# Kernel optimization log

Measured on AMD Instinct MI355X. Metric: run time of the kernel, lower is better.

## Reference

```python
import jax, jax.numpy as jnp
import numpy as np

B, TQ, TK = 2, 2048, 2048
H, E, D = 16, 256, 4096       # num_heads, embed_dim, d_model
DH = D // H                   # head_dim == embed_dim (required by per-head RMSNorm(embed_dim))
LAMBDA_INIT = 0.8
LAYER_INDEX = 0
EPS = 1.1920929e-07           # torch RMSNorm default eps = finfo(float32).eps


def setup_inputs() -> dict:
    key = jax.random.key(0)
    ks = jax.random.split(key, 14)
    s = 0.02
    lam_init_val = LAMBDA_INIT - 0.6 * float(np.exp(-0.3 * LAYER_INDEX))
    return {
        "x": jax.random.normal(ks[0], (B, TQ, E), jnp.float32),
        "encoder_out": jax.random.normal(ks[1], (B, TK, E), jnp.float32),
        "Wq": jax.random.normal(ks[2], (H, E, DH), jnp.float32) * s,
        "bq": jnp.zeros((H, DH), jnp.float32),
        "Wk": jax.random.normal(ks[3], (H, E, DH), jnp.float32) * s,
        "bk": jnp.zeros((H, DH), jnp.float32),
        "Wv": jax.random.normal(ks[4], (H, E, DH), jnp.float32) * s,
        "bv": jnp.zeros((H, DH), jnp.float32),
        "lq1": jax.random.normal(ks[5], (H, DH), jnp.float32) * 0.1,
        "lk1": jax.random.normal(ks[6], (H, DH), jnp.float32) * 0.1,
        "lq2": jax.random.normal(ks[7], (H, DH), jnp.float32) * 0.1,
        "lk2": jax.random.normal(ks[8], (H, DH), jnp.float32) * 0.1,
        "lam_init": jnp.full((H,), lam_init_val, jnp.float32),
        "g": jnp.ones((H, DH), jnp.float32),     # per-head RMSNorm weight
        "Wo": jax.random.normal(ks[9], (D, E), jnp.float32) * s,
        "bo": jnp.zeros((E,), jnp.float32),
    }


def reference(x, encoder_out, Wq, bq, Wk, bk, Wv, bv,
              lq1, lk1, lq2, lk2, lam_init, g, Wo, bo):
    # per-head projections, vectorized over heads: [B,H,T,DH]
    q = jnp.einsum('bte,hed->bhtd', x, Wq) + bq[:, None, :]
    k = jnp.einsum('bse,hed->bhsd', encoder_out, Wk) + bk[:, None, :]
    v = jnp.einsum('bse,hed->bhsd', encoder_out, Wv) + bv[:, None, :]
    dh2 = DH // 2
    q1, q2 = q[..., :dh2], q[..., dh2:]
    k1, k2 = k[..., :dh2], k[..., dh2:]
    scale = 1.0 / jnp.sqrt(jnp.float32(dh2))
    s1 = jax.nn.softmax(jnp.einsum('bhtd,bhsd->bhts', q1, k1) * scale, axis=-1)
    s2 = jax.nn.softmax(jnp.einsum('bhtd,bhsd->bhts', q2, k2) * scale, axis=-1)
    # learned per-head lambda scalar
    lam = jnp.exp(jnp.sum(lq1 * lk1, axis=-1)) - jnp.exp(jnp.sum(lq2 * lk2, axis=-1)) + lam_init  # [H]
    w = s1 - lam[None, :, None, None] * s2
    o = jnp.einsum('bhts,bhsd->bhtd', w, v)
    # per-head RMSNorm + (1 - lambda_init) scaling
    rms = jnp.sqrt(jnp.mean(o * o, axis=-1, keepdims=True) + EPS)
    o = (1.0 - LAMBDA_INIT) * (o / rms) * g[None, :, None, :]
    # concat heads -> output projection
    o = o.transpose(0, 2, 1, 3).reshape(B, TQ, D)
    return o @ Wo + bo
```

## Files before the change

### kernel.cpp

```cpp
#include <hip/hip_runtime.h>
#include <hip/hip_bf16.h>
#include <stdint.h>
#include <math.h>

typedef __bf16 bf16;
typedef __bf16 bf16x8 __attribute__((ext_vector_type(8)));
typedef float f32x4 __attribute__((ext_vector_type(4)));
typedef float f32x16 __attribute__((ext_vector_type(16)));
typedef unsigned int u32;

#define MFMA16(a, b, c) __builtin_amdgcn_mfma_f32_16x16x32_bf16(a, b, c, 0, 0, 0)
#define MFMA32(a, b, c) __builtin_amdgcn_mfma_f32_32x32x16_bf16(a, b, c, 0, 0, 0)

typedef const u32 __attribute__((address_space(1)))* gptr1;
typedef u32 __attribute__((address_space(3)))* lptr3;

__device__ __forceinline__ void load_lds16(const void* g, void* l) {
    __builtin_amdgcn_global_load_lds((gptr1)g, (lptr3)l, 16, 0, 0);
}

__device__ __forceinline__ u32 pk2(float lo, float hi_) {
    union { bf16 h[2]; u32 u; } t;
    t.h[0] = (bf16)lo; t.h[1] = (bf16)hi_;
    return t.u;
}

#define SCALE_QK 0.08838834764831845f
#define LOG2E 1.4426950408889634f
#define QK_PRESCALE (SCALE_QK * LOG2E)
#define RMS_EPS 1.1920929e-07f
#define OUT_SCALE 0.2f
#define M0_BIAS (-16.0f)

__global__ void cvt_act(const float* __restrict__ x, const float* __restrict__ enc,
                        bf16* __restrict__ xb, bf16* __restrict__ eb) {
    int gid = blockIdx.x * 256 + threadIdx.x;
    const float* src = (gid < 131072) ? x : enc;
    bf16* dst = (gid < 131072) ? xb : eb;
    int i = (gid & 131071) * 8;
    float4 v0 = *(const float4*)(src + i);
    float4 v1 = *(const float4*)(src + i + 4);
    union { bf16 h[8]; uint4 u; } p;
    p.h[0] = (bf16)v0.x; p.h[1] = (bf16)v0.y; p.h[2] = (bf16)v0.z; p.h[3] = (bf16)v0.w;
    p.h[4] = (bf16)v1.x; p.h[5] = (bf16)v1.y; p.h[6] = (bf16)v1.z; p.h[7] = (bf16)v1.w;
    *(uint4*)(dst + i) = p.u;
}

__global__ void txp_w(const float* __restrict__ Wq, const float* __restrict__ Wk,
                      const float* __restrict__ Wv,
                      bf16* __restrict__ WTq, bf16* __restrict__ WTk, bf16* __restrict__ WTv) {
    int z = blockIdx.z; int iw = z >> 4, hh = z & 15;
    const float* src = (iw == 0 ? Wq : iw == 1 ? Wk : Wv) + hh * 65536;
    bf16* dst = (iw == 0 ? WTq : iw == 1 ? WTk : WTv) + hh * 65536;
    __shared__ bf16 T[64][68];
    int r0 = blockIdx.y * 64, c0 = blockIdx.x * 64;
    int tid = threadIdx.x;
#pragma unroll
    for (int t = 0; t < 4; ++t) {
        int idx = tid + t * 256;
        int row = idx >> 4, c4 = (idx & 15) * 4;
        float4 v = *(const float4*)(src + (r0 + row) * 256 + c0 + c4);
        T[row][c4] = (bf16)v.x; T[row][c4 + 1] = (bf16)v.y;
        T[row][c4 + 2] = (bf16)v.z; T[row][c4 + 3] = (bf16)v.w;
    }
    __syncthreads();
#pragma unroll
    for (int t = 0; t < 2; ++t) {
        int idx = tid + t * 256;
        int crow = idx >> 3, r8 = (idx & 7) * 8;
        union { bf16 h[8]; uint4 u; } p;
#pragma unroll
        for (int j = 0; j < 8; ++j) p.h[j] = T[r8 + j][crow];
        *(uint4*)(dst + (c0 + crow) * 256 + r0 + r8) = p.u;
    }
}

__global__ void txp_wo(const float* __restrict__ Wo, bf16* __restrict__ WoT) {
    __shared__ bf16 T[64][68];
    int r0 = blockIdx.y * 64, c0 = blockIdx.x * 64;
    int tid = threadIdx.x;
#pragma unroll
    for (int t = 0; t < 4; ++t) {
        int idx = tid + t * 256;
        int row = idx >> 4, c4 = (idx & 15) * 4;
        float4 v = *(const float4*)(Wo + (size_t)(r0 + row) * 256 + c0 + c4);
        T[row][c4] = (bf16)v.x; T[row][c4 + 1] = (bf16)v.y;
        T[row][c4 + 2] = (bf16)v.z; T[row][c4 + 3] = (bf16)v.w;
    }
    __syncthreads();
#pragma unroll
    for (int t = 0; t < 2; ++t) {
        int idx = tid + t * 256;
        int crow = idx >> 3, r8 = (idx & 7) * 8;
        union { bf16 h[8]; uint4 u; } p;
#pragma unroll
        for (int j = 0; j < 8; ++j) p.h[j] = T[r8 + j][crow];
        *(uint4*)(WoT + (size_t)(c0 + crow) * 4096 + r0 + r8) = p.u;
    }
}

__global__ void lam_kernel(const float* __restrict__ lq1, const float* __restrict__ lk1,
                           const float* __restrict__ lq2, const float* __restrict__ lk2,
                           const float* __restrict__ lam_init, float* __restrict__ lam_out) {
    int tid = threadIdx.x; int hh = tid >> 4, i = tid & 15;
    float s1 = 0.f, s2 = 0.f;
#pragma unroll
    for (int j = 0; j < 16; ++j) {
        int d = i + j * 16;
        s1 += lq1[hh * 256 + d] * lk1[hh * 256 + d];
        s2 += lq2[hh * 256 + d] * lk2[hh * 256 + d];
    }
#pragma unroll
    for (int msk = 1; msk < 16; msk <<= 1) { s1 += __shfl_xor(s1, msk); s2 += __shfl_xor(s2, msk); }
    if (i == 0) lam_out[hh] = __expf(s1) - __expf(s2) + lam_init[hh];
}

__global__ __launch_bounds__(256) void proj_gemm(
    const bf16* __restrict__ xb, const bf16* __restrict__ eb,
    const bf16* __restrict__ WTq, const bf16* __restrict__ WTk, const bf16* __restrict__ WTv,
    const float* __restrict__ bq, const float* __restrict__ bk, const float* __restrict__ bv,
    bf16* __restrict__ Qb, bf16* __restrict__ Kb, bf16* __restrict__ VTb) {
    int z = blockIdx.z;
    const bf16* A = (z == 0) ? xb : eb;
    const bf16* BT = (z == 0) ? WTq : (z == 1) ? WTk : WTv;
    const float* bias = (z == 0) ? bq : (z == 1) ? bk : bv;
    bf16* out = (z == 0) ? Qb : Kb;
    float qs = (z == 0) ? QK_PRESCALE : 1.0f;

    __shared__ alignas(16) bf16 As[128 * 32];
    __shared__ alignas(16) bf16 Bs[128 * 32];
    int m0 = blockIdx.x * 128, n0 = blockIdx.y * 128;
    int tid = threadIdx.x, w = tid >> 6, lane = tid & 63;
    int lrow = lane & 15, lgrp = lane >> 4, lk8 = lgrp * 8;
    int wr = (w >> 1) * 64, wc = (w & 1) * 64;

    f32x4 acc[4][4];
#pragma unroll
    for (int i = 0; i < 4; ++i)
#pragma unroll
        for (int j = 0; j < 4; ++j) acc[i][j] = (f32x4){0.f, 0.f, 0.f, 0.f};

    for (int k0 = 0; k0 < 256; k0 += 32) {
        __syncthreads();
#pragma unroll
        for (int t = 0; t < 2; ++t) {
            int c = tid + t * 256;
            int row = c >> 2, k8 = (c & 3) * 8;
            load_lds16(A + (m0 + row) * 256 + k0 + k8, &As[c * 8]);
            load_lds16(BT + (n0 + row) * 256 + k0 + k8, &Bs[c * 8]);
        }
        __syncthreads();
        bf16x8 af[4], bfr[4];
#pragma unroll
        for (int f = 0; f < 4; ++f) af[f] = *(const bf16x8*)&As[(wr + f * 16 + lrow) * 32 + lk8];
#pragma unroll
        for (int f = 0; f < 4; ++f) bfr[f] = *(const bf16x8*)&Bs[(wc + f * 16 + lrow) * 32 + lk8];
#pragma unroll
        for (int i = 0; i < 4; ++i)
#pragma unroll
            for (int j = 0; j < 4; ++j) acc[i][j] = MFMA16(af[i], bfr[j], acc[i][j]);
    }

    if (z == 2) {
        int lg2 = ((lgrp & 1) << 1) | (lgrp >> 1);
#pragma unroll
        for (int i = 0; i < 4; ++i) {
            int m_ = m0 + wr + i * 16;
            int bb = m_ >> 11, tb = m_ & 2047;
#pragma unroll
            for (int j = 0; j < 4; ++j) {
                int n = n0 + wc + j * 16 + lrow;
                float bvv = bias[n];
                int hh = n >> 8, d = n & 255;
                union { bf16 h[4]; uint2 u2; } pk;
#pragma unroll
                for (int r = 0; r < 4; ++r) pk.h[r] = (bf16)(acc[i][j][r] + bvv);
                *(uint2*)(VTb + (((size_t)bb * 16 + hh) * 256 + d) * 2048 + tb + lg2 * 4) = pk.u2;
            }
        }
    } else {
#pragma unroll
        for (int i = 0; i < 4; ++i) {
#pragma unroll
            for (int j = 0; j < 4; ++j) {
                int n = n0 + wc + j * 16 + lrow;
                float bvv = bias[n];
                int hh = n >> 8, d = n & 255;
#pragma unroll
                for (int r = 0; r < 4; ++r) {
                    int m = m0 + wr + i * 16 + lgrp * 4 + r;
                    int bb = m >> 11, tt = m & 2047;
                    out[(((size_t)bb * 16 + hh) * 2048 + tt) * 256 + d] = (bf16)((acc[i][j][r] + bvv) * qs);
                }
            }
        }
    }
}

__global__ __launch_bounds__(512, 1) void attn_kernel(
    const bf16* __restrict__ Qb, const bf16* __restrict__ Kb, const bf16* __restrict__ VTb,
    const float* __restrict__ lam_ws, const float* __restrict__ g, bf16* __restrict__ On) {
    __shared__ alignas(16) char SMEM[140800];
    bf16* KsB = (bf16*)SMEM;
    bf16* VsB = (bf16*)(SMEM + 65536);
    float* o2buf  = (float*)SMEM;
    float* smem_i = (float*)(SMEM + 131072);
    float* smem_r = (float*)(SMEM + 132096);
    float* psum   = (float*)(SMEM + 132352);

    int orig = blockIdx.x;
    int xcd = orig & 7, idx = orig >> 3;
    int bh = xcd * 4 + (idx >> 4);
    int qb = idx & 15;
    int b = bh >> 4, h = bh & 15;

    int tid = threadIdx.x, w = tid >> 6, lane = tid & 63;
    int lq = lane & 31, hi = lane >> 5;
    int br = (w >> 1) & 1, qw = (w & 1) * 32, qh = w >> 2;
    int q0 = qb * 128 + qh * 64;
    int ksw = lq & 7;
    int vsw = (lq >> 1) & 3;

    const bf16* Qg = Qb + ((size_t)bh * 2048 + q0 + qw + lq) * 256 + br * 128;
    bf16x8 qf[8];
#pragma unroll
    for (int dk = 0; dk < 8; ++dk)
        qf[dk] = *(const bf16x8*)(Qg + dk * 16 + hi * 8);

    f32x16 o[8];
#pragma unroll
    for (int dt = 0; dt < 8; ++dt)
#pragma unroll
        for (int i = 0; i < 16; ++i) o[dt][i] = 0.f;
    float lsum = 0.f;

    const bf16* Kg = Kb + (size_t)bh * 2048 * 256;
    const bf16* VTg = VTb + (size_t)bh * 256 * 2048;

    auto STAGE = [&](int buf, int kt) {
        int s0 = kt * 32;
#pragma unroll
        for (int i = 0; i < 2; ++i) {
            int s = i * 512 + tid;
            int row = s >> 5;
            int cg = (s & 31) ^ (row & 7);
            load_lds16(Kg + (size_t)(s0 + row) * 256 + cg * 8, KsB + buf * 8192 + s * 8);
        }
#pragma unroll
        for (int i = 0; i < 2; ++i) {
            int s = i * 512 + tid;
            int row = s >> 2;
            int cg = (s & 3) ^ ((row >> 1) & 3);
            load_lds16(VTg + (size_t)row * 2048 + s0 + cg * 8, VsB + buf * 8192 + s * 8);
        }
    };

    STAGE(0, 0);
    STAGE(1, 1);
    STAGE(2, 2);

    for (int kt = 0; kt < 64; ++kt) {
        if (kt < 62)       asm volatile("s_waitcnt vmcnt(8)\ns_barrier" ::: "memory");
        else if (kt == 62) asm volatile("s_waitcnt vmcnt(4)\ns_barrier" ::: "memory");
        else               asm volatile("s_waitcnt vmcnt(0)\ns_barrier" ::: "memory");
        if (kt + 3 < 64) STAGE((kt + 3) & 3, kt + 3);

        const bf16* Kbuf = KsB + (kt & 3) * 8192;
        const bf16* Vbuf = VsB + (kt & 3) * 8192;

        f32x16 sa, sb;
#pragma unroll
        for (int i = 0; i < 16; ++i) { sa[i] = M0_BIAS; sb[i] = 0.f; }
        __builtin_amdgcn_s_setprio(1);
#pragma unroll
        for (int dk = 0; dk < 4; ++dk) {
            bf16x8 k0 = *(const bf16x8*)&Kbuf[lq * 256 + (((br * 16 + 4 * dk + hi) ^ ksw) << 3)];
            bf16x8 k1 = *(const bf16x8*)&Kbuf[lq * 256 + (((br * 16 + 4 * dk + 2 + hi) ^ ksw) << 3)];
            sa = MFMA32(k0, qf[2 * dk], sa);
            sb = MFMA32(k1, qf[2 * dk + 1], sb);
        }
        __builtin_amdgcn_s_setprio(0);

        float p[16];
        float ls0 = 0.f, ls1 = 0.f;
#pragma unroll
        for (int i = 0; i < 8; ++i) { p[i] = exp2f(sa[i] + sb[i]); ls0 += p[i]; }
#pragma unroll
        for (int i = 8; i < 16; ++i) { p[i] = exp2f(sa[i] + sb[i]); ls1 += p[i]; }
        lsum += ls0 + ls1;

        union { u32 u[4]; bf16x8 v; } PA0, PA1;
        PA0.u[0] = pk2(p[0], p[1]);   PA0.u[1] = pk2(p[2], p[3]);
        PA0.u[2] = pk2(p[4], p[5]);   PA0.u[3] = pk2(p[6], p[7]);
        PA1.u[0] = pk2(p[8], p[9]);   PA1.u[1] = pk2(p[10], p[11]);
        PA1.u[2] = pk2(p[12], p[13]); PA1.u[3] = pk2(p[14], p[15]);

        __builtin_amdgcn_s_setprio(1);
#pragma unroll
        for (int dt = 0; dt < 8; ++dt) {
            const bf16* vrow = &Vbuf[(dt * 32 + lq) * 32];
            bf16x8 v0 = *(const bf16x8*)&vrow[(hi ^ vsw) << 3];
            o[dt] = MFMA32(PA0.v, v0, o[dt]);
            bf16x8 v1 = *(const bf16x8*)&vrow[((2 + hi) ^ vsw) << 3];
            o[dt] = MFMA32(PA1.v, v1, o[dt]);
        }
        __builtin_amdgcn_s_setprio(0);
    }
    __syncthreads();

    lsum += __shfl_xor(lsum, 32);
    float lam = lam_ws[h];
    float inv = (br == 0) ? 1.f / lsum : lam / lsum;
    smem_i[br * 128 + qh * 64 + qw + lq] = inv;
    __syncthreads();

    float gv[8];
#pragma unroll
    for (int dt = 0; dt < 8; ++dt) gv[dt] = g[h * 256 + dt * 32 + lq] * OUT_SCALE;

    for (int hp = 0; hp < 2; ++hp) {
        if (qh == hp && br == 1) {
#pragma unroll
            for (int r = 0; r < 16; ++r) {
                int qp = (r & 3) + 8 * (r >> 2) + 4 * hi + qw;
                float i2 = smem_i[128 + qh * 64 + qp];
#pragma unroll
                for (int dt = 0; dt < 8; ++dt)
                    o2buf[qp * 256 + dt * 32 + lq] = o[dt][r] * i2;
            }
        }
        __syncthreads();
        if (qh == hp && br == 0) {
#pragma unroll
            for (int r = 0; r < 16; ++r) {
                int qp = (r & 3) + 8 * (r >> 2) + 4 * hi + qw;
                float i1 = smem_i[qh * 64 + qp];
                float ss = 0.f;
#pragma unroll
                for (int dt = 0; dt < 8; ++dt) {
                    float v = o[dt][r] * i1 - o2buf[qp * 256 + dt * 32 + lq];
                    o[dt][r] = v;
                    ss += v * v;
                }
                psum[qp * 33 + lq] = ss;
            }
        }
        __syncthreads();
        if (tid < 64) {
            float s = 0.f;
#pragma unroll
            for (int i = 0; i < 32; ++i) s += psum[tid * 33 + i];
            smem_r[tid] = 1.f / sqrtf(s * (1.f / 256.f) + RMS_EPS);
        }
        __syncthreads();
        if (qh == hp && br == 0) {
#pragma unroll
            for (int r = 0; r < 16; ++r) {
                int qp = (r & 3) + 8 * (r >> 2) + 4 * hi + qw;
                float rv = smem_r[qp];
                size_t base = ((size_t)b * 2048 + q0 + qp) * 4096 + h * 256;
#pragma unroll
                for (int dt = 0; dt < 8; ++dt)
                    On[base + dt * 32 + lq] = (bf16)(o[dt][r] * rv * gv[dt]);
            }
        }
        __syncthreads();
    }
}

__global__ __launch_bounds__(256) void out_gemm(const bf16* __restrict__ A, const bf16* __restrict__ BT,
                                                const float* __restrict__ bo, float* __restrict__ out) {
    __shared__ alignas(16) bf16 As[64 * 32];
    __shared__ alignas(16) bf16 Bs[64 * 32];
    int m0 = blockIdx.x * 64, n0 = blockIdx.y * 64;
    int tid = threadIdx.x, w = tid >> 6, lane = tid & 63;
    int lrow = lane & 15, lgrp = lane >> 4, lk8 = lgrp * 8;
    int wr = (w >> 1) * 32, wc = (w & 1) * 32;
    f32x4 acc[2][2];
#pragma unroll
    for (int i = 0; i < 2; ++i)
#pragma unroll
        for (int j = 0; j < 2; ++j) acc[i][j] = (f32x4){0.f, 0.f, 0.f, 0.f};
    for (int k0 = 0; k0 < 4096; k0 += 32) {
        __syncthreads();
        int row = tid >> 2, k8 = (tid & 3) * 8;
        load_lds16(A + (size_t)(m0 + row) * 4096 + k0 + k8, &As[tid * 8]);
        load_lds16(BT + (size_t)(n0 + row) * 4096 + k0 + k8, &Bs[tid * 8]);
        __syncthreads();
        bf16x8 af[2], bfr[2];
#pragma unroll
        for (int f = 0; f < 2; ++f) {
            af[f] = *(const bf16x8*)&As[(wr + f * 16 + lrow) * 32 + lk8];
            bfr[f] = *(const bf16x8*)&Bs[(wc + f * 16 + lrow) * 32 + lk8];
        }
#pragma unroll
        for (int i = 0; i < 2; ++i)
#pragma unroll
            for (int j = 0; j < 2; ++j) acc[i][j] = MFMA16(af[i], bfr[j], acc[i][j]);
    }
#pragma unroll
    for (int i = 0; i < 2; ++i)
#pragma unroll
        for (int j = 0; j < 2; ++j) {
            int n = n0 + wc + j * 16 + lrow;
            float bv = bo[n];
#pragma unroll
            for (int r = 0; r < 4; ++r) {
                int m = m0 + wr + i * 16 + lgrp * 4 + r;
                out[(size_t)m * 256 + n] = acc[i][j][r] + bv;
            }
        }
}

extern "C" void kernel_launch(void* const* d_in, const int* in_sizes, int n_in,
                              void* d_out, int out_size, void* d_ws, size_t ws_size,
                              hipStream_t stream) {
    const float* x = (const float*)d_in[0];
    const float* enc = (const float*)d_in[1];
    const float* Wq = (const float*)d_in[2];
    const float* bq = (const float*)d_in[3];
    const float* Wk = (const float*)d_in[4];
    const float* bk = (const float*)d_in[5];
    const float* Wv = (const float*)d_in[6];
    const float* bv = (const float*)d_in[7];
    const float* lq1 = (const float*)d_in[8];
    const float* lk1 = (const float*)d_in[9];
    const float* lq2 = (const float*)d_in[10];
    const float* lk2 = (const float*)d_in[11];
    const float* lam_init = (const float*)d_in[12];
    const float* g = (const float*)d_in[13];
    const float* Wo = (const float*)d_in[14];
    const float* bo = (const float*)d_in[15];
    float* out = (float*)d_out;

    char* ws = (char*)d_ws;
    const size_t MB = 1024 * 1024;
    bf16* xb  = (bf16*)(ws + 0 * MB);
    bf16* eb  = (bf16*)(ws + 2 * MB);
    bf16* WTq = (bf16*)(ws + 4 * MB);
    bf16* WTk = (bf16*)(ws + 6 * MB);
    bf16* WTv = (bf16*)(ws + 8 * MB);
    bf16* WoT = (bf16*)(ws + 10 * MB);
    float* lam = (float*)(ws + 12 * MB);
    bf16* Qb  = (bf16*)(ws + 13 * MB);
    bf16* Kb  = (bf16*)(ws + 45 * MB);
    bf16* On  = (bf16*)(ws + 77 * MB);
    bf16* VTb = (bf16*)(ws + 109 * MB);

    hipLaunchKernelGGL(cvt_act, dim3(1024), dim3(256), 0, stream, x, enc, xb, eb);
    hipLaunchKernelGGL(txp_w, dim3(4, 4, 48), dim3(256), 0, stream, Wq, Wk, Wv, WTq, WTk, WTv);
    hipLaunchKernelGGL(txp_wo, dim3(4, 64, 1), dim3(256), 0, stream, Wo, WoT);
    hipLaunchKernelGGL(lam_kernel, dim3(1), dim3(256), 0, stream, lq1, lk1, lq2, lk2, lam_init, lam);
    hipLaunchKernelGGL(proj_gemm, dim3(32, 32, 3), dim3(256), 0, stream,
                       xb, eb, WTq, WTk, WTv, bq, bk, bv, Qb, Kb, VTb);
    hipLaunchKernelGGL(attn_kernel, dim3(512), dim3(512), 0, stream, Qb, Kb, VTb, lam, g, On);
    hipLaunchKernelGGL(out_gemm, dim3(64, 4), dim3(256), 0, stream, On, WoT, bo, out);
}
```

Baseline: 343.1 us.

## Software-pipeline QK^T of the next tile ahead of the current tile's softmax and PV

Restructures the attention loop so the QK^T MFMAs for tile kt+1 are issued before the exp2/pack and PV MFMAs of tile kt. Score accumulators are double-buffered across an unrolled pair of tiles, and the wait count is tightened so only the next tile must have landed. The aim is to hide the exponential and packing latency behind matrix-core work. The cost is 32 extra live accumulator registers, which may affect occupancy, plus one redundant QK^T on the final tile.

```diff
diff --git a/kernel.cpp b/kernel.cpp
--- a/kernel.cpp
+++ b/kernel.cpp
@@ -255,38 +255,36 @@
         }
     };
 
-    STAGE(0, 0);
-    STAGE(1, 1);
-    STAGE(2, 2);
-
-    for (int kt = 0; kt < 64; ++kt) {
-        if (kt < 62)       asm volatile("s_waitcnt vmcnt(8)\ns_barrier" ::: "memory");
-        else if (kt == 62) asm volatile("s_waitcnt vmcnt(4)\ns_barrier" ::: "memory");
-        else               asm volatile("s_waitcnt vmcnt(0)\ns_barrier" ::: "memory");
-        if (kt + 3 < 64) STAGE((kt + 3) & 3, kt + 3);
-
-        const bf16* Kbuf = KsB + (kt & 3) * 8192;
-        const bf16* Vbuf = VsB + (kt & 3) * 8192;
-
-        f32x16 sa, sb;
-#pragma unroll
-        for (int i = 0; i < 16; ++i) { sa[i] = M0_BIAS; sb[i] = 0.f; }
+    auto QKT = [&](int kt_, f32x16& xa, f32x16& xb) {
+        const bf16* Kbuf = KsB + (kt_ & 3) * 8192;
+#pragma unroll
+        for (int i = 0; i < 16; ++i) { xa[i] = M0_BIAS; xb[i] = 0.f; }
         __builtin_amdgcn_s_setprio(1);
 #pragma unroll
         for (int dk = 0; dk < 4; ++dk) {
             bf16x8 k0 = *(const bf16x8*)&Kbuf[lq * 256 + (((br * 16 + 4 * dk + hi) ^ ksw) << 3)];
             bf16x8 k1 = *(const bf16x8*)&Kbuf[lq * 256 + (((br * 16 + 4 * dk + 2 + hi) ^ ksw) << 3)];
-            sa = MFMA32(k0, qf[2 * dk], sa);
-            sb = MFMA32(k1, qf[2 * dk + 1], sb);
+            xa = MFMA32(k0, qf[2 * dk], xa);
+            xb = MFMA32(k1, qf[2 * dk + 1], xb);
         }
         __builtin_amdgcn_s_setprio(0);
+    };
+
+    auto TILE = [&](int kt, f32x16& ca, f32x16& cb, f32x16& na_, f32x16& nb_) {
+        if (kt < 62) asm volatile("s_waitcnt vmcnt(4)" ::: "memory");
+        else         asm volatile("s_waitcnt vmcnt(0)" ::: "memory");
+        __builtin_amdgcn_s_barrier();
+        if (kt + 3 < 64) STAGE((kt + 3) & 3, kt + 3);
+
+        int nt = (kt + 1 < 64) ? kt + 1 : 63;
+        QKT(nt, na_, nb_);
 
         float p[16];
         float ls0 = 0.f, ls1 = 0.f;
 #pragma unroll
-        for (int i = 0; i < 8; ++i) { p[i] = exp2f(sa[i] + sb[i]); ls0 += p[i]; }
-#pragma unroll
-        for (int i = 8; i < 16; ++i) { p[i] = exp2f(sa[i] + sb[i]); ls1 += p[i]; }
+        for (int i = 0; i < 8; ++i) { p[i] = exp2f(ca[i] + cb[i]); ls0 += p[i]; }
+#pragma unroll
+        for (int i = 8; i < 16; ++i) { p[i] = exp2f(ca[i] + cb[i]); ls1 += p[i]; }
         lsum += ls0 + ls1;
 
         union { u32 u[4]; bf16x8 v; } PA0, PA1;
@@ -295,6 +293,7 @@
         PA1.u[0] = pk2(p[8], p[9]);   PA1.u[1] = pk2(p[10], p[11]);
         PA1.u[2] = pk2(p[12], p[13]); PA1.u[3] = pk2(p[14], p[15]);
 
+        const bf16* Vbuf = VsB + (kt & 3) * 8192;
         __builtin_amdgcn_s_setprio(1);
 #pragma unroll
         for (int dt = 0; dt < 8; ++dt) {
@@ -305,6 +304,20 @@
             o[dt] = MFMA32(PA1.v, v1, o[dt]);
         }
         __builtin_amdgcn_s_setprio(0);
+    };
+
+    STAGE(0, 0);
+    STAGE(1, 1);
+    STAGE(2, 2);
+    asm volatile("s_waitcnt vmcnt(8)" ::: "memory");
+    __builtin_amdgcn_s_barrier();
+
+    f32x16 sa0, sb0, sa1, sb1;
+    QKT(0, sa0, sb0);
+
+    for (int kt = 0; kt < 64; kt += 2) {
+        TILE(kt,     sa0, sb0, sa1, sb1);
+        TILE(kt + 1, sa1, sb1, sa0, sb0);
     }
     __syncthreads();
 
```

Measured after the change: 483.9 us. 41.0% more time.
